# Kernel optimization log

Hardware: AMD Instinct MI355X
Metric: run time of the kernel (lower is better)

Reference implementation:

```python
import jax, jax.numpy as jnp
import numpy as np

B, T, F = 8192, 30, 16
H1, H2 = 64, 32


def _lstm(x, Wih, Whh, b):
    """PyTorch-convention LSTM (gate order i,f,g,o). x: [B,T,I] -> (ys [B,T,H], hT [B,H])."""
    H = Whh.shape[1]
    h0 = jnp.zeros((x.shape[0], H), x.dtype)

    def step(carry, xt):
        h, c = carry
        z = xt @ Wih.T + h @ Whh.T + b  # [B,4H]
        i, f, g, o = jnp.split(z, 4, axis=-1)
        c = jax.nn.sigmoid(f) * c + jax.nn.sigmoid(i) * jnp.tanh(g)
        h = jax.nn.sigmoid(o) * jnp.tanh(c)
        return (h, c), h

    (hT, _), ys = jax.lax.scan(step, (h0, h0), jnp.swapaxes(x, 0, 1))
    return jnp.swapaxes(ys, 0, 1), hT


def setup_inputs() -> dict:
    key = jax.random.key(0)
    ks = jax.random.split(key, 16)
    s = 0.1  # small init scale for numerical sanity
    return {
        "x": jax.random.normal(ks[0], (B, T, F), jnp.float32),
        "Wih1": jax.random.normal(ks[1], (4 * H1, F), jnp.float32) * s,
        "Whh1": jax.random.normal(ks[2], (4 * H1, H1), jnp.float32) * s,
        "b1": jax.random.normal(ks[3], (4 * H1,), jnp.float32) * s,
        "Wih2": jax.random.normal(ks[4], (4 * H2, H1), jnp.float32) * s,
        "Whh2": jax.random.normal(ks[5], (4 * H2, H2), jnp.float32) * s,
        "b2": jax.random.normal(ks[6], (4 * H2,), jnp.float32) * s,
        "Wih3": jax.random.normal(ks[7], (4 * H2, H2), jnp.float32) * s,
        "Whh3": jax.random.normal(ks[8], (4 * H2, H2), jnp.float32) * s,
        "b3": jax.random.normal(ks[9], (4 * H2,), jnp.float32) * s,
        "Wih4": jax.random.normal(ks[10], (4 * H1, H2), jnp.float32) * s,
        "Whh4": jax.random.normal(ks[11], (4 * H1, H1), jnp.float32) * s,
        "b4": jax.random.normal(ks[12], (4 * H1,), jnp.float32) * s,
        "Wout": jax.random.normal(ks[13], (F, H1), jnp.float32) * s,
        "bout": jax.random.normal(ks[14], (F,), jnp.float32) * s,
    }


def reference(x, Wih1, Whh1, b1, Wih2, Whh2, b2, Wih3, Whh3, b3, Wih4, Whh4, b4, Wout, bout):
    ys1, _ = _lstm(x, Wih1, Whh1, b1)          # encoder LSTM(64)
    _, latent = _lstm(ys1, Wih2, Whh2, b2)      # encoder LSTM(32) -> final hidden [B,32]
    repeated = jnp.broadcast_to(latent[:, None, :], (latent.shape[0], T, latent.shape[1]))
    ys3, _ = _lstm(repeated, Wih3, Whh3, b3)    # decoder LSTM(32)
    ys4, _ = _lstm(ys3, Wih4, Whh4, b4)         # decoder LSTM(64)
    return ys4 @ Wout.T + bout                  # [B,T,F]
```

## Files before the change

kernel.cpp:

```cpp
#include <hip/hip_runtime.h>


#define TT 30
#define FF 16
#define NT 384

typedef unsigned short u16t;
typedef __attribute__((ext_vector_type(8))) short short8;
typedef __attribute__((ext_vector_type(4))) short short4v;
typedef __attribute__((ext_vector_type(4))) float floatx4;

#define MFMA(a, b, c) __builtin_amdgcn_mfma_f32_16x16x32_bf16(a, b, c, 0, 0, 0)

#if __has_builtin(__builtin_amdgcn_exp2f)
#define EXP2(x) __builtin_amdgcn_exp2f(x)
#else
#define EXP2(x) exp2f(x)
#endif

template <int P> struct IC { static constexpr int v = P; };

__device__ __forceinline__ float rcpf(float v) { return __builtin_amdgcn_rcpf(v); }
__device__ __forceinline__ u16t f2bf(float f) {
  unsigned int u = __float_as_uint(f);
  u = (u + 0x7FFFu + ((u >> 16) & 1u)) >> 16;
  return (u16t)u;
}
__device__ __forceinline__ short8 ldFragS(const float* p, float s) {
  const float4 lo = *(const float4*)p;
  const float4 hi = *(const float4*)(p + 4);
  short8 r;
  r[0] = (short)f2bf(lo.x * s); r[1] = (short)f2bf(lo.y * s);
  r[2] = (short)f2bf(lo.z * s); r[3] = (short)f2bf(lo.w * s);
  r[4] = (short)f2bf(hi.x * s); r[5] = (short)f2bf(hi.y * s);
  r[6] = (short)f2bf(hi.z * s); r[7] = (short)f2bf(hi.w * s);
  return r;
}
__device__ __forceinline__ float cellUp(const floatx4 acc, float& c) {
  float ei = EXP2(-acc[0]);
  float ef = EXP2(-acc[1]);
  float eg = EXP2(-acc[2]);
  float eo = EXP2(-acc[3]);
  float fv = rcpf(1.f + ef);
  float P  = (1.f - eg) * rcpf((1.f + ei) * (1.f + eg));
  c = fv * c + P;
  float ec = EXP2(-2.885390082f * c);
  return (1.f - ec) * rcpf((1.f + eo) * (1.f + ec));
}

__global__ __launch_bounds__(NT, 3) void lstm_ae_mfma9(
    const float* __restrict__ x,
    const float* __restrict__ Wih1, const float* __restrict__ Whh1, const float* __restrict__ b1,
    const float* __restrict__ Wih2, const float* __restrict__ Whh2, const float* __restrict__ b2,
    const float* __restrict__ Wih3, const float* __restrict__ Whh3, const float* __restrict__ b3,
    const float* __restrict__ Wih4, const float* __restrict__ Whh4, const float* __restrict__ b4,
    const float* __restrict__ Wout, const float* __restrict__ bout,
    float* __restrict__ out)
{
  __shared__ __align__(16) u16t xAll[16 * 968];
  __shared__ __align__(16) u16t aB[16 * 264];

  const int t = threadIdx.x;
  const int w = t >> 6, lane = t & 63;
  const int q = lane >> 4, n = lane & 15;
  const int q8 = q * 8;
  const int bBase = blockIdx.x * 16;
  const int nlo = n >> 2, ngt = n & 3;
  const int r0 = n * 264;
  const int x0 = n * 968;
  const bool isZ1 = (w < 4);
  const int u = w & 1;

  const float L1 = 1.442695041f, L2 = 2.885390082f;
  const float sA = (ngt == 2) ? L2 : L1;

  for (int i = t; i < 16 * 264; i += NT) aB[i] = 0;
  {
    const float* xb = x + (size_t)bBase * (TT * FF);
    for (int i4 = t; i4 < 1920; i4 += NT) {
      int e = i4 * 4;
      int b = e / 480, r = e - b * 480;
      int stp = r >> 4, f = r & 15;
      float4 v = *(const float4*)&xb[e];
      short4v s4 = { (short)f2bf(v.x), (short)f2bf(v.y), (short)f2bf(v.z), (short)f2bf(v.w) };
      *(short4v*)&xAll[b * 968 + stp * 32 + f] = s4;
    }
    for (int i = t; i < 7680; i += NT) {
      int b = i / 480, r = i - b * 480;
      int stp = r >> 4, f = r & 15;
      xAll[b * 968 + stp * 32 + 16 + f] = 0;
    }
  }
  const short8 z8 = { 0, 0, 0, 0, 0, 0, 0, 0 };
  short8 wAf[4][3]; floatx4 biasA[4];
  if (isZ1) {
#pragma unroll
    for (int tt = 0; tt < 4; ++tt) {
      int T = w + 4 * tt;
      int row = ngt * 64 + T * 4 + nlo;
      wAf[tt][0] = z8;
      if (q < 2) wAf[tt][0] = ldFragS(&Wih1[row * 16 + q8], sA);
      wAf[tt][1] = ldFragS(&Whh1[row * 64 + q8], sA);
      wAf[tt][2] = ldFragS(&Whh1[row * 64 + 32 + q8], sA);
#pragma unroll
      for (int r = 0; r < 4; ++r) biasA[tt][r] = b1[r * 64 + T * 4 + q] * (r == 2 ? L2 : L1);
    }
  } else {
#pragma unroll
    for (int tt = 0; tt < 4; ++tt) {
      int T = 4 * u + tt;
      int row = ngt * 32 + T * 4 + nlo;
      wAf[tt][0] = ldFragS(&Wih2[row * 64 + q8], sA);
      wAf[tt][1] = ldFragS(&Wih2[row * 64 + 32 + q8], sA);
      wAf[tt][2] = ldFragS(&Whh2[row * 32 + q8], sA);
#pragma unroll
      for (int r = 0; r < 4; ++r) biasA[tt][r] = b2[r * 32 + T * 4 + q] * (r == 2 ? L2 : L1);
    }
  }
  __syncthreads();

  float cA[4] = {0.f, 0.f, 0.f, 0.f};
  short8 bxN;

  if (isZ1) {
    const short8 bx0 = *(const short8*)&xAll[x0 + q8];
#pragma unroll
    for (int tt = 0; tt < 4; ++tt) {
      floatx4 a = biasA[tt];
      a = MFMA(wAf[tt][0], bx0, a);
      aB[r0 + (w + 4 * tt) * 4 + q] = f2bf(cellUp(a, cA[tt]));
    }
    bxN = *(const short8*)&xAll[x0 + 32 + q8];
  }
  __syncthreads();

  auto stepA = [&](int st, auto pc) {
    constexpr int p = decltype(pc)::v;
    const short8 h1a = *(const short8*)&aB[r0 + p * 64 + q8];
    const short8 h1b = *(const short8*)&aB[r0 + p * 64 + 32 + q8];
    if (isZ1) {
#pragma unroll
      for (int tt = 0; tt < 4; ++tt) {
        floatx4 a = biasA[tt];
        a = MFMA(wAf[tt][0], bxN, a);
        a = MFMA(wAf[tt][1], h1a, a);
        a = MFMA(wAf[tt][2], h1b, a);
        aB[r0 + (1 - p) * 64 + (w + 4 * tt) * 4 + q] = f2bf(cellUp(a, cA[tt]));
      }
      const int nx = (st + 2 < TT) ? st + 2 : TT - 1;
      bxN = *(const short8*)&xAll[x0 + nx * 32 + q8];
    } else {
      const short8 h2 = *(const short8*)&aB[r0 + 128 + (1 - p) * 32 + q8];
#pragma unroll
      for (int tt = 0; tt < 4; ++tt) {
        floatx4 a = biasA[tt];
        a = MFMA(wAf[tt][0], h1a, a);
        a = MFMA(wAf[tt][1], h1b, a);
        a = MFMA(wAf[tt][2], h2, a);
        aB[r0 + 128 + p * 32 + (4 * u + tt) * 4 + q] = f2bf(cellUp(a, cA[tt]));
      }
    }
    __syncthreads();
  };
  for (int st = 0; st < 28; st += 2) { stepA(st, IC<0>{}); stepA(st + 1, IC<1>{}); }
  stepA(28, IC<0>{});
  if (!isZ1) {
    const short8 h1a = *(const short8*)&aB[r0 + 64 + q8];
    const short8 h1b = *(const short8*)&aB[r0 + 96 + q8];
    const short8 h2  = *(const short8*)&aB[r0 + 128 + q8];
#pragma unroll
    for (int tt = 0; tt < 4; ++tt) {
      floatx4 a = biasA[tt];
      a = MFMA(wAf[tt][0], h1a, a);
      a = MFMA(wAf[tt][1], h1b, a);
      a = MFMA(wAf[tt][2], h2, a);
      aB[r0 + 160 + (4 * u + tt) * 4 + q] = f2bf(cellUp(a, cA[tt]));
    }
  }
  __syncthreads();

  short8 wBf[4][3]; floatx4 biasB[4];
  short8 wof[2]; floatx4 biasO;
  short8 blat;
  if (isZ1) {
#pragma unroll
    for (int tt = 0; tt < 4; ++tt) {
      int T = w + 4 * tt;
      int row = ngt * 64 + T * 4 + nlo;
      wBf[tt][0] = ldFragS(&Wih4[row * 32 + q8], sA);
      wBf[tt][1] = ldFragS(&Whh4[row * 64 + q8], sA);
      wBf[tt][2] = ldFragS(&Whh4[row * 64 + 32 + q8], sA);
#pragma unroll
      for (int r = 0; r < 4; ++r) biasB[tt][r] = b4[r * 64 + T * 4 + q] * (r == 2 ? L2 : L1);
    }
    wof[0] = ldFragS(&Wout[n * 64 + q8], 1.f);
    wof[1] = ldFragS(&Wout[n * 64 + 32 + q8], 1.f);
    biasO = *(const floatx4*)&bout[q * 4];
  } else {
#pragma unroll
    for (int tt = 0; tt < 4; ++tt) {
      int T = 4 * u + tt;
      int row = ngt * 32 + T * 4 + nlo;
      wBf[tt][0] = ldFragS(&Wih3[row * 32 + q8], sA);
      wBf[tt][1] = ldFragS(&Whh3[row * 32 + q8], sA);
#pragma unroll
      for (int r = 0; r < 4; ++r) biasB[tt][r] = b3[r * 32 + T * 4 + q] * (r == 2 ? L2 : L1);
    }
    blat = *(const short8*)&aB[r0 + 160 + q8];
  }
  for (int i = t; i < 1024; i += NT) aB[(i >> 6) * 264 + 64 + (i & 63)] = 0;
  __syncthreads();

  float cB[4] = {0.f, 0.f, 0.f, 0.f};

  if (!isZ1) {
#pragma unroll
    for (int tt = 0; tt < 4; ++tt) {
      floatx4 a = biasB[tt];
      a = MFMA(wBf[tt][0], blat, a);
      aB[r0 + 192 + (4 * u + tt) * 4 + q] = f2bf(cellUp(a, cB[tt]));
    }
  }
  __syncthreads();

  auto stepB = [&](int st, auto pc) {
    constexpr int p = decltype(pc)::v;
    const short8 h3 = *(const short8*)&aB[r0 + 192 + p * 32 + q8];
    if (isZ1) {
      const short8 h4a = *(const short8*)&aB[r0 + (1 - p) * 64 + q8];
      const short8 h4b = *(const short8*)&aB[r0 + (1 - p) * 64 + 32 + q8];
#pragma unroll
      for (int tt = 0; tt < 4; ++tt) {
        floatx4 a = biasB[tt];
        a = MFMA(wBf[tt][0], h3, a);
        a = MFMA(wBf[tt][1], h4a, a);
        a = MFMA(wBf[tt][2], h4b, a);
        aB[r0 + p * 64 + (w + 4 * tt) * 4 + q] = f2bf(cellUp(a, cB[tt]));
      }
      if (st > 0 && w == ((st - 1) & 3)) {
        floatx4 y = biasO;
        y = MFMA(wof[0], h4a, y);
        y = MFMA(wof[1], h4b, y);
        *(floatx4*)&out[((size_t)(bBase + n) * TT + (st - 1)) * FF + q * 4] = y;
      }
    } else {
#pragma unroll
      for (int tt = 0; tt < 4; ++tt) {
        floatx4 a = biasB[tt];
        a = MFMA(wBf[tt][0], blat, a);
        a = MFMA(wBf[tt][1], h3, a);
        aB[r0 + 192 + (1 - p) * 32 + (4 * u + tt) * 4 + q] = f2bf(cellUp(a, cB[tt]));
      }
    }
    __syncthreads();
  };
  for (int st = 0; st < 28; st += 2) { stepB(st, IC<0>{}); stepB(st + 1, IC<1>{}); }
  stepB(28, IC<0>{});
  if (isZ1) {
    const short8 h3  = *(const short8*)&aB[r0 + 224 + q8];
    const short8 h4a = *(const short8*)&aB[r0 + q8];
    const short8 h4b = *(const short8*)&aB[r0 + 32 + q8];
#pragma unroll
    for (int tt = 0; tt < 4; ++tt) {
      floatx4 a = biasB[tt];
      a = MFMA(wBf[tt][0], h3, a);
      a = MFMA(wBf[tt][1], h4a, a);
      a = MFMA(wBf[tt][2], h4b, a);
      aB[r0 + 64 + (w + 4 * tt) * 4 + q] = f2bf(cellUp(a, cB[tt]));
    }
    if (w == 0) {
      floatx4 y = biasO;
      y = MFMA(wof[0], h4a, y);
      y = MFMA(wof[1], h4b, y);
      *(floatx4*)&out[((size_t)(bBase + n) * TT + 28) * FF + q * 4] = y;
    }
  }
  __syncthreads();
  if (w == 1) {
    const short8 ba = *(const short8*)&aB[r0 + 64 + q8];
    const short8 bb = *(const short8*)&aB[r0 + 96 + q8];
    floatx4 y = biasO;
    y = MFMA(wof[0], ba, y);
    y = MFMA(wof[1], bb, y);
    *(floatx4*)&out[((size_t)(bBase + n) * TT + 29) * FF + q * 4] = y;
  }
}

extern "C" void kernel_launch(void* const* d_in, const int* in_sizes, int n_in,
                              void* d_out, int out_size, void* d_ws, size_t ws_size,
                              hipStream_t stream) {
  const float* x    = (const float*)d_in[0];
  const float* Wih1 = (const float*)d_in[1];
  const float* Whh1 = (const float*)d_in[2];
  const float* b1   = (const float*)d_in[3];
  const float* Wih2 = (const float*)d_in[4];
  const float* Whh2 = (const float*)d_in[5];
  const float* b2   = (const float*)d_in[6];
  const float* Wih3 = (const float*)d_in[7];
  const float* Whh3 = (const float*)d_in[8];
  const float* b3   = (const float*)d_in[9];
  const float* Wih4 = (const float*)d_in[10];
  const float* Whh4 = (const float*)d_in[11];
  const float* b4   = (const float*)d_in[12];
  const float* Wout = (const float*)d_in[13];
  const float* bout = (const float*)d_in[14];
  float* out = (float*)d_out;

  const int B = in_sizes[0] / (TT * FF);
  dim3 grid(B / 16), block(NT);
  lstm_ae_mfma9<<<grid, block, 0, stream>>>(
      x, Wih1, Whh1, b1, Wih2, Whh2, b2, Wih3, Whh3, b3,
      Wih4, Whh4, b4, Wout, bout, out);
}
```

Baseline: 192.0 us.

## Double block to 32 batch rows with 12 waves and cheaper LSTM step

Doubles the block to 768 threads covering 32 batch rows, so each wave pair handles two 16-row halves and fewer blocks are launched. Several smaller changes come with it. The cell update is rewritten to use one reciprocal for the c update. Hidden values are converted with a packed bf16 convert instruction. Barriers become an LDS-only waitcnt plus s_barrier, and the decoder's constant Wih3·latent term is precomputed once into an accumulator. The cost is doubled LDS per block, which may reduce occupancy, and 8192/32 = 256 blocks may leave the 256-CU device thinly loaded.

```diff
diff --git a/kernel.cpp b/kernel.cpp
--- a/kernel.cpp
+++ b/kernel.cpp
@@ -3,7 +3,7 @@
 
 #define TT 30
 #define FF 16
-#define NT 384
+#define NT 768
 
 typedef unsigned short u16t;
 typedef __attribute__((ext_vector_type(8))) short short8;
@@ -25,6 +25,15 @@
   unsigned int u = __float_as_uint(f);
   u = (u + 0x7FFFu + ((u >> 16) & 1u)) >> 16;
   return (u16t)u;
+}
+__device__ __forceinline__ unsigned int pkbf(float a, float b) {
+  unsigned int r;
+  asm("v_cvt_pk_bf16_f32 %0, %1, %2" : "=v"(r) : "v"(a), "v"(b));
+  return r;
+}
+__device__ __forceinline__ void barLDS() {
+  asm volatile("s_waitcnt lgkmcnt(0)" ::: "memory");
+  __builtin_amdgcn_s_barrier();
 }
 __device__ __forceinline__ short8 ldFragS(const float* p, float s) {
   const float4 lo = *(const float4*)p;
@@ -41,14 +50,15 @@
   float ef = EXP2(-acc[1]);
   float eg = EXP2(-acc[2]);
   float eo = EXP2(-acc[3]);
-  float fv = rcpf(1.f + ef);
-  float P  = (1.f - eg) * rcpf((1.f + ei) * (1.f + eg));
-  c = fv * c + P;
+  float pig = (1.f + ei) * (1.f + eg);
+  float pf  = 1.f + ef;
+  float num = c * pig + (1.f - eg) * pf;
+  c = num * rcpf(pf * pig);
   float ec = EXP2(-2.885390082f * c);
   return (1.f - ec) * rcpf((1.f + eo) * (1.f + ec));
 }
 
-__global__ __launch_bounds__(NT, 3) void lstm_ae_mfma9(
+__global__ __launch_bounds__(NT, 3) void lstm_ae_mfma12(
     const float* __restrict__ x,
     const float* __restrict__ Wih1, const float* __restrict__ Whh1, const float* __restrict__ b1,
     const float* __restrict__ Wih2, const float* __restrict__ Whh2, const float* __restrict__ b2,
@@ -57,27 +67,29 @@
     const float* __restrict__ Wout, const float* __restrict__ bout,
     float* __restrict__ out)
 {
-  __shared__ __align__(16) u16t xAll[16 * 968];
-  __shared__ __align__(16) u16t aB[16 * 264];
+  __shared__ __align__(16) u16t xAll[32 * 968];
+  __shared__ __align__(16) u16t aB[32 * 264];
 
   const int t = threadIdx.x;
   const int w = t >> 6, lane = t & 63;
   const int q = lane >> 4, n = lane & 15;
   const int q8 = q * 8;
-  const int bBase = blockIdx.x * 16;
+  const int bBase = blockIdx.x * 32;
   const int nlo = n >> 2, ngt = n & 3;
-  const int r0 = n * 264;
-  const int x0 = n * 968;
-  const bool isZ1 = (w < 4);
-  const int u = w & 1;
+  const bool isZ1 = (w < 8);
+  const int hf = w & 1;
+  const int jA = w >> 1;
+  const int j2 = (w >> 1) - 4;
+  const int rh = (n + 16 * hf) * 264;
+  const int xh = (n + 16 * hf) * 968;
 
   const float L1 = 1.442695041f, L2 = 2.885390082f;
   const float sA = (ngt == 2) ? L2 : L1;
 
-  for (int i = t; i < 16 * 264; i += NT) aB[i] = 0;
+  for (int i = t; i < 32 * 264; i += NT) aB[i] = 0;
   {
     const float* xb = x + (size_t)bBase * (TT * FF);
-    for (int i4 = t; i4 < 1920; i4 += NT) {
+    for (int i4 = t; i4 < 3840; i4 += NT) {
       int e = i4 * 4;
       int b = e / 480, r = e - b * 480;
       int stp = r >> 4, f = r & 15;
@@ -85,7 +97,7 @@
       short4v s4 = { (short)f2bf(v.x), (short)f2bf(v.y), (short)f2bf(v.z), (short)f2bf(v.w) };
       *(short4v*)&xAll[b * 968 + stp * 32 + f] = s4;
     }
-    for (int i = t; i < 7680; i += NT) {
+    for (int i = t; i < 15360; i += NT) {
       int b = i / 480, r = i - b * 480;
       int stp = r >> 4, f = r & 15;
       xAll[b * 968 + stp * 32 + 16 + f] = 0;
@@ -96,7 +108,7 @@
   if (isZ1) {
 #pragma unroll
     for (int tt = 0; tt < 4; ++tt) {
-      int T = w + 4 * tt;
+      int T = jA + 4 * tt;
       int row = ngt * 64 + T * 4 + nlo;
       wAf[tt][0] = z8;
       if (q < 2) wAf[tt][0] = ldFragS(&Wih1[row * 16 + q8], sA);
@@ -108,7 +120,7 @@
   } else {
 #pragma unroll
     for (int tt = 0; tt < 4; ++tt) {
-      int T = 4 * u + tt;
+      int T = j2 + 2 * tt;
       int row = ngt * 32 + T * 4 + nlo;
       wAf[tt][0] = ldFragS(&Wih2[row * 64 + q8], sA);
       wAf[tt][1] = ldFragS(&Wih2[row * 64 + 32 + q8], sA);
@@ -121,23 +133,30 @@
 
   float cA[4] = {0.f, 0.f, 0.f, 0.f};
   short8 bxN;
+  float hv[4];
 
   if (isZ1) {
-    const short8 bx0 = *(const short8*)&xAll[x0 + q8];
+    const short8 bx0 = *(const short8*)&xAll[xh + q8];
 #pragma unroll
     for (int tt = 0; tt < 4; ++tt) {
       floatx4 a = biasA[tt];
       a = MFMA(wAf[tt][0], bx0, a);
-      aB[r0 + (w + 4 * tt) * 4 + q] = f2bf(cellUp(a, cA[tt]));
-    }
-    bxN = *(const short8*)&xAll[x0 + 32 + q8];
-  }
-  __syncthreads();
+      hv[tt] = cellUp(a, cA[tt]);
+    }
+    unsigned int pk01 = pkbf(hv[0], hv[1]);
+    unsigned int pk23 = pkbf(hv[2], hv[3]);
+    aB[rh + (jA + 0) * 4 + q] = (u16t)pk01;
+    aB[rh + (jA + 4) * 4 + q] = (u16t)(pk01 >> 16);
+    aB[rh + (jA + 8) * 4 + q] = (u16t)pk23;
+    aB[rh + (jA + 12) * 4 + q] = (u16t)(pk23 >> 16);
+    bxN = *(const short8*)&xAll[xh + 32 + q8];
+  }
+  barLDS();
 
   auto stepA = [&](int st, auto pc) {
     constexpr int p = decltype(pc)::v;
-    const short8 h1a = *(const short8*)&aB[r0 + p * 64 + q8];
-    const short8 h1b = *(const short8*)&aB[r0 + p * 64 + 32 + q8];
+    const short8 h1a = *(const short8*)&aB[rh + p * 64 + q8];
+    const short8 h1b = *(const short8*)&aB[rh + p * 64 + 32 + q8];
     if (isZ1) {
 #pragma unroll
       for (int tt = 0; tt < 4; ++tt) {
@@ -145,47 +164,65 @@
         a = MFMA(wAf[tt][0], bxN, a);
         a = MFMA(wAf[tt][1], h1a, a);
         a = MFMA(wAf[tt][2], h1b, a);
-        aB[r0 + (1 - p) * 64 + (w + 4 * tt) * 4 + q] = f2bf(cellUp(a, cA[tt]));
-      }
+        hv[tt] = cellUp(a, cA[tt]);
+      }
+      unsigned int pk01 = pkbf(hv[0], hv[1]);
+      unsigned int pk23 = pkbf(hv[2], hv[3]);
+      aB[rh + (1 - p) * 64 + (jA + 0) * 4 + q] = (u16t)pk01;
+      aB[rh + (1 - p) * 64 + (jA + 4) * 4 + q] = (u16t)(pk01 >> 16);
+      aB[rh + (1 - p) * 64 + (jA + 8) * 4 + q] = (u16t)pk23;
+      aB[rh + (1 - p) * 64 + (jA + 12) * 4 + q] = (u16t)(pk23 >> 16);
       const int nx = (st + 2 < TT) ? st + 2 : TT - 1;
-      bxN = *(const short8*)&xAll[x0 + nx * 32 + q8];
+      bxN = *(const short8*)&xAll[xh + nx * 32 + q8];
     } else {
-      const short8 h2 = *(const short8*)&aB[r0 + 128 + (1 - p) * 32 + q8];
+      const short8 h2 = *(const short8*)&aB[rh + 128 + (1 - p) * 32 + q8];
 #pragma unroll
       for (int tt = 0; tt < 4; ++tt) {
         floatx4 a = biasA[tt];
         a = MFMA(wAf[tt][0], h1a, a);
         a = MFMA(wAf[tt][1], h1b, a);
         a = MFMA(wAf[tt][2], h2, a);
-        aB[r0 + 128 + p * 32 + (4 * u + tt) * 4 + q] = f2bf(cellUp(a, cA[tt]));
-      }
-    }
-    __syncthreads();
+        hv[tt] = cellUp(a, cA[tt]);
+      }
+      unsigned int pk01 = pkbf(hv[0], hv[1]);
+      unsigned int pk23 = pkbf(hv[2], hv[3]);
+      aB[rh + 128 + p * 32 + (j2 + 0) * 4 + q] = (u16t)pk01;
+      aB[rh + 128 + p * 32 + (j2 + 2) * 4 + q] = (u16t)(pk01 >> 16);
+      aB[rh + 128 + p * 32 + (j2 + 4) * 4 + q] = (u16t)pk23;
+      aB[rh + 128 + p * 32 + (j2 + 6) * 4 + q] = (u16t)(pk23 >> 16);
+    }
+    barLDS();
   };
   for (int st = 0; st < 28; st += 2) { stepA(st, IC<0>{}); stepA(st + 1, IC<1>{}); }
   stepA(28, IC<0>{});
   if (!isZ1) {
-    const short8 h1a = *(const short8*)&aB[r0 + 64 + q8];
-    const short8 h1b = *(const short8*)&aB[r0 + 96 + q8];
-    const short8 h2  = *(const short8*)&aB[r0 + 128 + q8];
+    const short8 h1a = *(const short8*)&aB[rh + 64 + q8];
+    const short8 h1b = *(const short8*)&aB[rh + 96 + q8];
+    const short8 h2  = *(const short8*)&aB[rh + 128 + q8];
 #pragma unroll
     for (int tt = 0; tt < 4; ++tt) {
       floatx4 a = biasA[tt];
       a = MFMA(wAf[tt][0], h1a, a);
       a = MFMA(wAf[tt][1], h1b, a);
       a = MFMA(wAf[tt][2], h2, a);
-      aB[r0 + 160 + (4 * u + tt) * 4 + q] = f2bf(cellUp(a, cA[tt]));
-    }
+      hv[tt] = cellUp(a, cA[tt]);
+    }
+    unsigned int pk01 = pkbf(hv[0], hv[1]);
+    unsigned int pk23 = pkbf(hv[2], hv[3]);
+    aB[rh + 160 + (j2 + 0) * 4 + q] = (u16t)pk01;
+    aB[rh + 160 + (j2 + 2) * 4 + q] = (u16t)(pk01 >> 16);
+    aB[rh + 160 + (j2 + 4) * 4 + q] = (u16t)pk23;
+    aB[rh + 160 + (j2 + 6) * 4 + q] = (u16t)(pk23 >> 16);
   }
   __syncthreads();
 
   short8 wBf[4][3]; floatx4 biasB[4];
   short8 wof[2]; floatx4 biasO;
-  short8 blat;
+  short8 w3h[4]; floatx4 acc3c[4];
   if (isZ1) {
 #pragma unroll
     for (int tt = 0; tt < 4; ++tt) {
-      int T = w + 4 * tt;
+      int T = jA + 4 * tt;
       int row = ngt * 64 + T * 4 + nlo;
       wBf[tt][0] = ldFragS(&Wih4[row * 32 + q8], sA);
       wBf[tt][1] = ldFragS(&Whh4[row * 64 + q8], sA);
@@ -197,92 +234,112 @@
     wof[1] = ldFragS(&Wout[n * 64 + 32 + q8], 1.f);
     biasO = *(const floatx4*)&bout[q * 4];
   } else {
-#pragma unroll
-    for (int tt = 0; tt < 4; ++tt) {
-      int T = 4 * u + tt;
+    const short8 blat = *(const short8*)&aB[rh + 160 + q8];
+#pragma unroll
+    for (int tt = 0; tt < 4; ++tt) {
+      int T = j2 + 2 * tt;
       int row = ngt * 32 + T * 4 + nlo;
-      wBf[tt][0] = ldFragS(&Wih3[row * 32 + q8], sA);
-      wBf[tt][1] = ldFragS(&Whh3[row * 32 + q8], sA);
-#pragma unroll
-      for (int r = 0; r < 4; ++r) biasB[tt][r] = b3[r * 32 + T * 4 + q] * (r == 2 ? L2 : L1);
-    }
-    blat = *(const short8*)&aB[r0 + 160 + q8];
-  }
-  for (int i = t; i < 1024; i += NT) aB[(i >> 6) * 264 + 64 + (i & 63)] = 0;
+      const short8 w3i = ldFragS(&Wih3[row * 32 + q8], sA);
+      w3h[tt] = ldFragS(&Whh3[row * 32 + q8], sA);
+      floatx4 b3v;
+#pragma unroll
+      for (int r = 0; r < 4; ++r) b3v[r] = b3[r * 32 + T * 4 + q] * (r == 2 ? L2 : L1);
+      acc3c[tt] = MFMA(w3i, blat, b3v);
+    }
+  }
+  for (int i = t; i < 2048; i += NT) aB[(i >> 6) * 264 + 64 + (i & 63)] = 0;
   __syncthreads();
 
   float cB[4] = {0.f, 0.f, 0.f, 0.f};
 
   if (!isZ1) {
 #pragma unroll
-    for (int tt = 0; tt < 4; ++tt) {
-      floatx4 a = biasB[tt];
-      a = MFMA(wBf[tt][0], blat, a);
-      aB[r0 + 192 + (4 * u + tt) * 4 + q] = f2bf(cellUp(a, cB[tt]));
-    }
-  }
-  __syncthreads();
+    for (int tt = 0; tt < 4; ++tt) hv[tt] = cellUp(acc3c[tt], cB[tt]);
+    unsigned int pk01 = pkbf(hv[0], hv[1]);
+    unsigned int pk23 = pkbf(hv[2], hv[3]);
+    aB[rh + 192 + (j2 + 0) * 4 + q] = (u16t)pk01;
+    aB[rh + 192 + (j2 + 2) * 4 + q] = (u16t)(pk01 >> 16);
+    aB[rh + 192 + (j2 + 4) * 4 + q] = (u16t)pk23;
+    aB[rh + 192 + (j2 + 6) * 4 + q] = (u16t)(pk23 >> 16);
+  }
+  barLDS();
 
   auto stepB = [&](int st, auto pc) {
     constexpr int p = decltype(pc)::v;
-    const short8 h3 = *(const short8*)&aB[r0 + 192 + p * 32 + q8];
+    const short8 h3 = *(const short8*)&aB[rh + 192 + p * 32 + q8];
     if (isZ1) {
-      const short8 h4a = *(const short8*)&aB[r0 + (1 - p) * 64 + q8];
-      const short8 h4b = *(const short8*)&aB[r0 + (1 - p) * 64 + 32 + q8];
+      const short8 h4a = *(const short8*)&aB[rh + (1 - p) * 64 + q8];
+      const short8 h4b = *(const short8*)&aB[rh + (1 - p) * 64 + 32 + q8];
 #pragma unroll
       for (int tt = 0; tt < 4; ++tt) {
         floatx4 a = biasB[tt];
         a = MFMA(wBf[tt][0], h3, a);
         a = MFMA(wBf[tt][1], h4a, a);
         a = MFMA(wBf[tt][2], h4b, a);
-        aB[r0 + p * 64 + (w + 4 * tt) * 4 + q] = f2bf(cellUp(a, cB[tt]));
-      }
-      if (st > 0 && w == ((st - 1) & 3)) {
+        hv[tt] = cellUp(a, cB[tt]);
+      }
+      unsigned int pk01 = pkbf(hv[0], hv[1]);
+      unsigned int pk23 = pkbf(hv[2], hv[3]);
+      aB[rh + p * 64 + (jA + 0) * 4 + q] = (u16t)pk01;
+      aB[rh + p * 64 + (jA + 4) * 4 + q] = (u16t)(pk01 >> 16);
+      aB[rh + p * 64 + (jA + 8) * 4 + q] = (u16t)pk23;
+      aB[rh + p * 64 + (jA + 12) * 4 + q] = (u16t)(pk23 >> 16);
+      if (st > 0 && jA == ((st - 1) & 3)) {
         floatx4 y = biasO;
         y = MFMA(wof[0], h4a, y);
         y = MFMA(wof[1], h4b, y);
-        *(floatx4*)&out[((size_t)(bBase + n) * TT + (st - 1)) * FF + q * 4] = y;
+        *(floatx4*)&out[((size_t)(bBase + n + 16 * hf) * TT + (st - 1)) * FF + q * 4] = y;
       }
     } else {
 #pragma unroll
       for (int tt = 0; tt < 4; ++tt) {
-        floatx4 a = biasB[tt];
-        a = MFMA(wBf[tt][0], blat, a);
-        a = MFMA(wBf[tt][1], h3, a);
-        aB[r0 + 192 + (1 - p) * 32 + (4 * u + tt) * 4 + q] = f2bf(cellUp(a, cB[tt]));
-      }
-    }
-    __syncthreads();
+        floatx4 a = MFMA(w3h[tt], h3, acc3c[tt]);
+        hv[tt] = cellUp(a, cB[tt]);
+      }
+      unsigned int pk01 = pkbf(hv[0], hv[1]);
+      unsigned int pk23 = pkbf(hv[2], hv[3]);
+      aB[rh + 192 + (1 - p) * 32 + (j2 + 0) * 4 + q] = (u16t)pk01;
+      aB[rh + 192 + (1 - p) * 32 + (j2 + 2) * 4 + q] = (u16t)(pk01 >> 16);
+      aB[rh + 192 + (1 - p) * 32 + (j2 + 4) * 4 + q] = (u16t)pk23;
+      aB[rh + 192 + (1 - p) * 32 + (j2 + 6) * 4 + q] = (u16t)(pk23 >> 16);
+    }
+    barLDS();
   };
   for (int st = 0; st < 28; st += 2) { stepB(st, IC<0>{}); stepB(st + 1, IC<1>{}); }
   stepB(28, IC<0>{});
   if (isZ1) {
-    const short8 h3  = *(const short8*)&aB[r0 + 224 + q8];
-    const short8 h4a = *(const short8*)&aB[r0 + q8];
-    const short8 h4b = *(const short8*)&aB[r0 + 32 + q8];
+    const short8 h3  = *(const short8*)&aB[rh + 224 + q8];
+    const short8 h4a = *(const short8*)&aB[rh + q8];
+    const short8 h4b = *(const short8*)&aB[rh + 32 + q8];
 #pragma unroll
     for (int tt = 0; tt < 4; ++tt) {
       floatx4 a = biasB[tt];
       a = MFMA(wBf[tt][0], h3, a);
       a = MFMA(wBf[tt][1], h4a, a);
       a = MFMA(wBf[tt][2], h4b, a);
-      aB[r0 + 64 + (w + 4 * tt) * 4 + q] = f2bf(cellUp(a, cB[tt]));
-    }
-    if (w == 0) {
+      hv[tt] = cellUp(a, cB[tt]);
+    }
+    unsigned int pk01 = pkbf(hv[0], hv[1]);
+    unsigned int pk23 = pkbf(hv[2], hv[3]);
+    aB[rh + 64 + (jA + 0) * 4 + q] = (u16t)pk01;
+    aB[rh + 64 + (jA + 4) * 4 + q] = (u16t)(pk01 >> 16);
+    aB[rh + 64 + (jA + 8) * 4 + q] = (u16t)pk23;
+    aB[rh + 64 + (jA + 12) * 4 + q] = (u16t)(pk23 >> 16);
+    if (jA == 0) {
       floatx4 y = biasO;
       y = MFMA(wof[0], h4a, y);
       y = MFMA(wof[1], h4b, y);
-      *(floatx4*)&out[((size_t)(bBase + n) * TT + 28) * FF + q * 4] = y;
-    }
-  }
-  __syncthreads();
-  if (w == 1) {
-    const short8 ba = *(const short8*)&aB[r0 + 64 + q8];
-    const short8 bb = *(const short8*)&aB[r0 + 96 + q8];
+      *(floatx4*)&out[((size_t)(bBase + n + 16 * hf) * TT + 28) * FF + q * 4] = y;
+    }
+  }
+  barLDS();
+  if (isZ1 && jA == 1) {
+    const short8 ba = *(const short8*)&aB[rh + 64 + q8];
+    const short8 bb = *(const short8*)&aB[rh + 96 + q8];
     floatx4 y = biasO;
     y = MFMA(wof[0], ba, y);
     y = MFMA(wof[1], bb, y);
-    *(floatx4*)&out[((size_t)(bBase + n) * TT + 29) * FF + q * 4] = y;
+    *(floatx4*)&out[((size_t)(bBase + n + 16 * hf) * TT + 29) * FF + q * 4] = y;
   }
 }
 
@@ -307,8 +364,8 @@
   float* out = (float*)d_out;
 
   const int B = in_sizes[0] / (TT * FF);
-  dim3 grid(B / 16), block(NT);
-  lstm_ae_mfma9<<<grid, block, 0, stream>>>(
+  dim3 grid(B / 32), block(NT);
+  lstm_ae_mfma12<<<grid, block, 0, stream>>>(
       x, Wih1, Whh1, b1, Wih2, Whh2, b2, Wih3, Whh3, b3,
       Wih4, Whh4, b4, Wout, bout, out);
 }
```

Result: faster. 161.4 us (-15.9%).
